# Kernel tuning notes

Measured on AMD Instinct MI355X. Metric: run time of the kernel, lower is better.

The kernel has to match this reference:

```python
import jax, jax.numpy as jnp
import numpy as np

N, IN_DIM, HID, HEADS = 4096, 256, 64, 8


def setup_inputs() -> dict:
    key = jax.random.key(0)
    ks = jax.random.split(key, 9)
    feats = jax.random.normal(ks[0], (N, IN_DIM), dtype=jnp.float32)
    adj = jax.random.bernoulli(ks[1], 0.01, (N, N)) | jnp.eye(N, dtype=bool)
    def lin(k, fin, fout):
        return jax.random.normal(k, (fin, fout), dtype=jnp.float32) / np.float32(np.sqrt(fin))
    return {
        "features": feats,
        "adjacency": adj,
        "W_in": lin(ks[2], IN_DIM, HID * HEADS),            # linear (no bias)
        "W_out": lin(ks[3], HID * HEADS, HID),              # out_proj
        "b_out": jnp.zeros((HID,), jnp.float32),
        "W_c1": lin(ks[4], HID * 2, HID),                   # classifier[1]
        "b_c1": jnp.zeros((HID,), jnp.float32),
        "W_c2": lin(ks[5], HID, 1),                         # classifier[3]
        "b_c2": jnp.zeros((1,), jnp.float32),
    }


def reference(features, adjacency, W_in, W_out, b_out, W_c1, b_c1, W_c2, b_c2):
    n = features.shape[0]
    # multi-head GAT: [H, N, D]
    proj = (features @ W_in).reshape(n, HEADS, HID).transpose(1, 0, 2)
    logits = jnp.einsum('hnd,hmd->hnm', proj, proj) / np.float32(np.sqrt(HID))
    logits = jnp.where(adjacency[None, :, :], logits, -jnp.inf)
    attn = jax.nn.softmax(logits, axis=-1)
    attended = jnp.einsum('hnm,hmd->hnd', attn, proj)
    attended = attended.transpose(1, 0, 2).reshape(n, HEADS * HID)
    node_states = attended @ W_out + b_out
    # memory_bank is None -> concat with zeros
    fused = jnp.concatenate([node_states, jnp.zeros_like(node_states)], axis=-1)
    h = jax.nn.gelu(fused, approximate=False) @ W_c1 + b_c1
    scores = (jax.nn.gelu(h, approximate=False) @ W_c2 + b_c2).squeeze(-1)
    # attention heatmap: masked row-normalized cosine similarity
    eps = np.float32(1e-8)
    norm = jnp.maximum(jnp.linalg.norm(node_states, axis=-1, keepdims=True), eps)
    xn = node_states / norm
    sim = jnp.where(adjacency, xn @ xn.T, 0.0)
    heatmap = sim / (sim.sum(axis=-1, keepdims=True) + eps)
    return scores, heatmap
```

## Files before the change

kernel.cpp:

```cpp
#include <hip/hip_runtime.h>
#include <math.h>

constexpr int NN    = 4096;
constexpr int INDIM = 256;
constexpr int HID   = 64;
constexpr int HEADS = 8;
constexpr int HH    = HID * HEADS;
constexpr int DMAX  = 256;
constexpr int PROJ_BLOCKS = 512;

typedef float        vfloat4 __attribute__((ext_vector_type(4)));
typedef unsigned int vuint4  __attribute__((ext_vector_type(4)));

__device__ __forceinline__ float gelu_exact(float x) {
    return 0.5f * x * (1.0f + erff(x * 0.70710678118654752f));
}

__device__ __forceinline__ float wave_reduce64(float v) {
    v += __shfl_xor(v, 32); v += __shfl_xor(v, 16); v += __shfl_xor(v, 8);
    v += __shfl_xor(v, 4);  v += __shfl_xor(v, 2);  v += __shfl_xor(v, 1);
    return v;
}

__global__ __launch_bounds__(256) void prep_kernel(
    const void* __restrict__ adjv,
    const float* __restrict__ A, const float* __restrict__ B,
    float* __restrict__ projT,
    unsigned short* __restrict__ nbr_g, int* __restrict__ deg_g) {
    __shared__ float Bs[64][64];
    __shared__ int wsum[4], u8w[4];
    const int pb = blockIdx.x, t = threadIdx.x;
    const int wv = t >> 6, lane = t & 63;

    if (pb < PROJ_BLOCKS) {
        const int bx = pb >> 6, by = pb & 63;
        const int tx = t & 15, ty = t >> 4;
        const float* ap0 = A + (size_t)(by * 64 + ty * 4 + 0) * INDIM;
        const float* ap1 = A + (size_t)(by * 64 + ty * 4 + 1) * INDIM;
        const float* ap2 = A + (size_t)(by * 64 + ty * 4 + 2) * INDIM;
        const float* ap3 = A + (size_t)(by * 64 + ty * 4 + 3) * INDIM;
        float acc[4][4] = {{0.0f}};

        for (int kq = 0; kq < 4; ++kq) {
            #pragma unroll
            for (int i = t; i < 64 * 16; i += 256) {
                const int k = i >> 4, c4 = (i & 15) * 4;
                *reinterpret_cast<float4*>(&Bs[k][c4]) =
                    *reinterpret_cast<const float4*>(
                        B + (size_t)(kq * 64 + k) * HH + bx * 64 + c4);
            }
            __syncthreads();
            #pragma unroll 2
            for (int k = 0; k < 64; k += 4) {
                const int ka = kq * 64 + k;
                float4 av[4];
                av[0] = *reinterpret_cast<const float4*>(ap0 + ka);
                av[1] = *reinterpret_cast<const float4*>(ap1 + ka);
                av[2] = *reinterpret_cast<const float4*>(ap2 + ka);
                av[3] = *reinterpret_cast<const float4*>(ap3 + ka);
                float4 bv[4];
                #pragma unroll
                for (int kk = 0; kk < 4; ++kk)
                    bv[kk] = *reinterpret_cast<const float4*>(&Bs[k + kk][tx * 4]);
                #pragma unroll
                for (int i = 0; i < 4; ++i) {
                    const float a0 = av[i].x, a1 = av[i].y, a2 = av[i].z, a3 = av[i].w;
                    acc[i][0] += a0 * bv[0].x + a1 * bv[1].x + a2 * bv[2].x + a3 * bv[3].x;
                    acc[i][1] += a0 * bv[0].y + a1 * bv[1].y + a2 * bv[2].y + a3 * bv[3].y;
                    acc[i][2] += a0 * bv[0].z + a1 * bv[1].z + a2 * bv[2].z + a3 * bv[3].z;
                    acc[i][3] += a0 * bv[0].w + a1 * bv[1].w + a2 * bv[2].w + a3 * bv[3].w;
                }
            }
            __syncthreads();
        }
        #pragma unroll
        for (int i = 0; i < 4; ++i) {
            float4 o = {acc[i][0], acc[i][1], acc[i][2], acc[i][3]};
            *reinterpret_cast<float4*>(
                projT + ((size_t)bx * NN + by * 64 + ty * 4 + i) * HID + tx * 4) = o;
        }
    } else {
        const int n = pb - PROJ_BLOCKS;
        const vuint4 r8 = __builtin_nontemporal_load(
            reinterpret_cast<const vuint4*>(
                (const unsigned char*)adjv + (size_t)n * NN + 16 * t));
        const vuint4 pw = *(reinterpret_cast<const vuint4*>(adjv) + t);
        int u8loc = 0;
        #pragma unroll
        for (int a = 0; a < 4; ++a) {
            const unsigned w = pw[a];
            if (((w & ~0x01010101u) == 0u) && ((w & 0xFFFFFF00u) != 0u)) u8loc = 1;
        }
        const unsigned long long wb = __ballot(u8loc);
        if (lane == 0) u8w[wv] = (wb != 0ull);
        __syncthreads();
        const bool isU8 = (u8w[0] | u8w[1] | u8w[2] | u8w[3]) != 0;

        unsigned int nzmask = 0;
        if (isU8) {
            #pragma unroll
            for (int a = 0; a < 4; ++a)
                #pragma unroll
                for (int j = 0; j < 4; ++j)
                    if ((r8[a] >> (8 * j)) & 0xFFu) nzmask |= 1u << (a * 4 + j);
        } else {
            const vuint4* p = reinterpret_cast<const vuint4*>(
                (const unsigned int*)adjv + (size_t)n * NN + 16 * t);
            #pragma unroll
            for (int a = 0; a < 4; ++a) {
                const vuint4 r = __builtin_nontemporal_load(p + a);
                if (r[0]) nzmask |= 1u << (a * 4 + 0);
                if (r[1]) nzmask |= 1u << (a * 4 + 1);
                if (r[2]) nzmask |= 1u << (a * 4 + 2);
                if (r[3]) nzmask |= 1u << (a * 4 + 3);
            }
        }
        const int c = __popc(nzmask);
        int x = c;
        #pragma unroll
        for (int d = 1; d < 64; d <<= 1) {
            int y = __shfl_up(x, d);
            if (lane >= d) x += y;
        }
        if (lane == 63) wsum[wv] = x;
        __syncthreads();
        int base = 0;
        #pragma unroll
        for (int i = 0; i < 4; ++i)
            if (i < wv) base += wsum[i];
        const int deg = min(wsum[0] + wsum[1] + wsum[2] + wsum[3], DMAX);
        if (t == 0) deg_g[n] = deg;
        int o = base + x - c;
        unsigned int mm = nzmask;
        while (mm) {
            const int j = __ffs(mm) - 1;
            mm &= mm - 1;
            if (o < DMAX) nbr_g[(size_t)n * DMAX + o] = (unsigned short)(16 * t + j);
            ++o;
        }
    }
}

__global__ __launch_bounds__(256) void attn_kernel(
    const float* __restrict__ projT,
    const unsigned short* __restrict__ nbr_g, const int* __restrict__ deg_g,
    float* __restrict__ attended) {
    __shared__ unsigned short nl[4][DMAX];
    const int b = blockIdx.x, t = threadIdx.x;
    const int wv = t >> 6, lane = t & 63;
    const int h = b & 7;
    const int n = (b >> 3) * 4 + wv;
    const int deg = deg_g[n];

    *reinterpret_cast<ushort4*>(&nl[wv][lane * 4]) =
        *reinterpret_cast<const ushort4*>(nbr_g + (size_t)n * DMAX + lane * 4);

    const float* tab = projT + (size_t)h * NN * HID;
    const int g = lane >> 3, dl = (lane & 7) * 8;

    float q[8];
    {
        const float4 a = *reinterpret_cast<const float4*>(tab + (size_t)n * HID + dl);
        const float4 bq = *reinterpret_cast<const float4*>(tab + (size_t)n * HID + dl + 4);
        q[0] = a.x;  q[1] = a.y;  q[2] = a.z;  q[3] = a.w;
        q[4] = bq.x; q[5] = bq.y; q[6] = bq.z; q[7] = bq.w;
    }

    float l = 0.0f;
    float acc[8] = {0.f, 0.f, 0.f, 0.f, 0.f, 0.f, 0.f, 0.f};
    for (int c0 = 0; c0 < deg; c0 += 8) {
        const int c = c0 + g;
        const int idx = nl[wv][min(c, deg - 1)];
        const float* kp = tab + (size_t)idx * HID + dl;
        const float4 ka = *reinterpret_cast<const float4*>(kp);
        const float4 kb = *reinterpret_cast<const float4*>(kp + 4);
        float kf[8] = {ka.x, ka.y, ka.z, ka.w, kb.x, kb.y, kb.z, kb.w};
        float s = q[0]*kf[0] + q[1]*kf[1] + q[2]*kf[2] + q[3]*kf[3] +
                  q[4]*kf[4] + q[5]*kf[5] + q[6]*kf[6] + q[7]*kf[7];
        s += __shfl_xor(s, 1); s += __shfl_xor(s, 2); s += __shfl_xor(s, 4);
        const float w = (c < deg) ? expf(s * 0.125f) : 0.0f;
        l += w;
        #pragma unroll
        for (int i = 0; i < 8; ++i) acc[i] += w * kf[i];
    }
    l += __shfl_xor(l, 8); l += __shfl_xor(l, 16); l += __shfl_xor(l, 32);
    #pragma unroll
    for (int i = 0; i < 8; ++i) {
        acc[i] += __shfl_xor(acc[i], 8);
        acc[i] += __shfl_xor(acc[i], 16);
        acc[i] += __shfl_xor(acc[i], 32);
    }
    const float invL = 1.0f / l;
    if (g == 0) {
        float4 o1 = {acc[0] * invL, acc[1] * invL, acc[2] * invL, acc[3] * invL};
        float4 o2 = {acc[4] * invL, acc[5] * invL, acc[6] * invL, acc[7] * invL};
        float* dst = attended + (size_t)n * HH + h * HID + dl;
        *reinterpret_cast<float4*>(dst)     = o1;
        *reinterpret_cast<float4*>(dst + 4) = o2;
    }
}

__global__ __launch_bounds__(256) void post_kernel(
    const float* __restrict__ attended,
    const float* __restrict__ W_out, const float* __restrict__ b_out,
    const float* __restrict__ W_c1, const float* __restrict__ b_c1,
    const float* __restrict__ W_c2, const float* __restrict__ b_c2,
    float* __restrict__ scores, float* __restrict__ xn) {
    __shared__ float qv2[4][HH];
    __shared__ float red[4][256];
    __shared__ float nsbuf[4][HID];
    const int n0 = blockIdx.x * 4, t = threadIdx.x;
    const int wv = t >> 6, lane = t & 63;

    #pragma unroll
    for (int nd = 0; nd < 4; ++nd) {
        qv2[nd][t]       = attended[(size_t)(n0 + nd) * HH + t];
        qv2[nd][t + 256] = attended[(size_t)(n0 + nd) * HH + t + 256];
    }
    __syncthreads();

    const int j = t & 63, part = t >> 6;
    float p0 = 0.f, p1 = 0.f, p2 = 0.f, p3 = 0.f;
    for (int d = part * 128; d < part * 128 + 128; ++d) {
        const float w = W_out[d * HID + j];
        p0 += qv2[0][d] * w; p1 += qv2[1][d] * w;
        p2 += qv2[2][d] * w; p3 += qv2[3][d] * w;
    }
    red[0][t] = p0; red[1][t] = p1; red[2][t] = p2; red[3][t] = p3;
    __syncthreads();
    if (wv < 4 && lane < HID) {
        nsbuf[wv][lane] = red[wv][lane] + red[wv][lane + 64] +
                          red[wv][lane + 128] + red[wv][lane + 192] + b_out[lane];
    }
    __syncthreads();

    const int n = n0 + wv;
    const float ns = nsbuf[wv][lane];
    const float s2 = wave_reduce64(ns * ns);
    const float invn = 1.0f / fmaxf(sqrtf(s2), 1e-8f);
    xn[(size_t)n * HID + lane] = ns * invn;
    const float gb = gelu_exact(ns);
    __syncthreads();
    nsbuf[wv][lane] = gb;
    float hv = b_c1[lane];
    for (int i = 0; i < HID; ++i) hv += nsbuf[wv][i] * W_c1[i * HID + lane];
    const float hb = gelu_exact(hv);
    const float sc_ = wave_reduce64(hb * W_c2[lane]);
    if (lane == 0) scores[n] = sc_ + b_c2[0];
}

__global__ __launch_bounds__(256, 8) void heat_kernel(
    const unsigned short* __restrict__ nbr_g, const int* __restrict__ deg_g,
    const float* __restrict__ xn, float* __restrict__ heat) {
    __shared__ float srow[NN];
    __shared__ float simv[DMAX];
    __shared__ unsigned short nl[DMAX];
    __shared__ float inv_s;
    const int n = blockIdx.x, t = threadIdx.x;
    const int wv = t >> 6, lane = t & 63;
    const int deg = deg_g[n];

    float4* sr4 = (float4*)srow;
    const float4 z4 = {0.f, 0.f, 0.f, 0.f};
    for (int i = t; i < NN / 4; i += 256) sr4[i] = z4;
    if (t < deg) nl[t] = nbr_g[(size_t)n * DMAX + t];
    const float xq = xn[(size_t)n * HID + lane];
    __syncthreads();

    for (int c = wv; c < deg; c += 4) {
        const int m = nl[c];
        float s = wave_reduce64(xq * xn[(size_t)m * HID + lane]);
        if (lane == 0) { srow[m] = s; simv[c] = s; }
    }
    __syncthreads();
    if (t < 64) {
        float ps = 0.0f;
        for (int c = t; c < deg; c += 64) ps += simv[c];
        ps = wave_reduce64(ps);
        if (t == 0) inv_s = 1.0f / (ps + 1e-8f);
    }
    __syncthreads();
    const float inv = inv_s;
    vfloat4* hr4 = (vfloat4*)(heat + (size_t)n * NN);
    for (int i = t; i < NN / 4; i += 256) {
        float4 v = sr4[i];
        vfloat4 nv = {v.x * inv, v.y * inv, v.z * inv, v.w * inv};
        __builtin_nontemporal_store(nv, hr4 + i);
    }
}

extern "C" void kernel_launch(void* const* d_in, const int* in_sizes, int n_in,
                              void* d_out, int out_size, void* d_ws, size_t ws_size,
                              hipStream_t stream) {
    const float* features = (const float*)d_in[0];
    const void*  adj      = d_in[1];
    const float* W_in     = (const float*)d_in[2];
    const float* W_out    = (const float*)d_in[3];
    const float* b_out    = (const float*)d_in[4];
    const float* W_c1     = (const float*)d_in[5];
    const float* b_c1     = (const float*)d_in[6];
    const float* W_c2     = (const float*)d_in[7];
    const float* b_c2     = (const float*)d_in[8];

    float* scores = (float*)d_out;
    float* heat   = (float*)d_out + NN;

    float*          projT    = (float*)d_ws;
    float*          attended = projT + (size_t)HEADS * NN * HID;
    float*          xn       = attended + (size_t)NN * HH;
    unsigned short* nbr_g    = (unsigned short*)(xn + (size_t)NN * HID);
    int*            deg_g    = (int*)(nbr_g + (size_t)NN * DMAX);

    prep_kernel<<<PROJ_BLOCKS + NN, 256, 0, stream>>>(adj, features, W_in,
                                                      projT, nbr_g, deg_g);
    attn_kernel<<<NN * HEADS / 4, 256, 0, stream>>>(projT, nbr_g, deg_g, attended);
    post_kernel<<<NN / 4, 256, 0, stream>>>(attended, W_out, b_out, W_c1, b_c1,
                                            W_c2, b_c2, scores, xn);
    heat_kernel<<<NN, 256, 0, stream>>>(nbr_g, deg_g, xn, heat);
}
```

Measured before the change: 220.4 us.

## Stage A tiles in LDS and register-prefetch next k-tile in projection GEMM

The projection GEMM in prep_kernel used to read A directly from global memory in the inner loop. It now stages the A tile in padded shared memory alongside B. The next k-slab of both A and B is prefetched into registers while the current slab is computed, so global load latency overlaps the FMAs. This costs extra LDS (about 17KB more) and register pressure, which could lower occupancy, and it only touches the projection part of a larger pipeline.

Result: slower. 225.1 us (+2.2%).

```diff
diff --git a/kernel.cpp b/kernel.cpp
--- a/kernel.cpp
+++ b/kernel.cpp
@@ -27,6 +27,7 @@
     const float* __restrict__ A, const float* __restrict__ B,
     float* __restrict__ projT,
     unsigned short* __restrict__ nbr_g, int* __restrict__ deg_g) {
+    __shared__ float As[64][68];
     __shared__ float Bs[64][64];
     __shared__ int wsum[4], u8w[4];
     const int pb = blockIdx.x, t = threadIdx.x;
@@ -35,30 +36,43 @@
     if (pb < PROJ_BLOCKS) {
         const int bx = pb >> 6, by = pb & 63;
         const int tx = t & 15, ty = t >> 4;
-        const float* ap0 = A + (size_t)(by * 64 + ty * 4 + 0) * INDIM;
-        const float* ap1 = A + (size_t)(by * 64 + ty * 4 + 1) * INDIM;
-        const float* ap2 = A + (size_t)(by * 64 + ty * 4 + 2) * INDIM;
-        const float* ap3 = A + (size_t)(by * 64 + ty * 4 + 3) * INDIM;
         float acc[4][4] = {{0.0f}};
 
+        float4 ar[4], br[4];
+        const int r_row[4] = {t >> 4, (t + 256) >> 4, (t + 512) >> 4, (t + 768) >> 4};
+        const int r_c4    = (t & 15) * 4;
+
+        #pragma unroll
+        for (int j = 0; j < 4; ++j) {
+            ar[j] = *reinterpret_cast<const float4*>(
+                A + (size_t)(by * 64 + r_row[j]) * INDIM + 0 * 64 + r_c4);
+            br[j] = *reinterpret_cast<const float4*>(
+                B + (size_t)(0 * 64 + r_row[j]) * HH + bx * 64 + r_c4);
+        }
+
         for (int kq = 0; kq < 4; ++kq) {
+            __syncthreads();
             #pragma unroll
-            for (int i = t; i < 64 * 16; i += 256) {
-                const int k = i >> 4, c4 = (i & 15) * 4;
-                *reinterpret_cast<float4*>(&Bs[k][c4]) =
-                    *reinterpret_cast<const float4*>(
-                        B + (size_t)(kq * 64 + k) * HH + bx * 64 + c4);
+            for (int j = 0; j < 4; ++j) {
+                *reinterpret_cast<float4*>(&As[r_row[j]][r_c4]) = ar[j];
+                *reinterpret_cast<float4*>(&Bs[r_row[j]][r_c4]) = br[j];
+            }
+            if (kq < 3) {
+                #pragma unroll
+                for (int j = 0; j < 4; ++j) {
+                    ar[j] = *reinterpret_cast<const float4*>(
+                        A + (size_t)(by * 64 + r_row[j]) * INDIM + (kq + 1) * 64 + r_c4);
+                    br[j] = *reinterpret_cast<const float4*>(
+                        B + (size_t)((kq + 1) * 64 + r_row[j]) * HH + bx * 64 + r_c4);
+                }
             }
             __syncthreads();
             #pragma unroll 2
             for (int k = 0; k < 64; k += 4) {
-                const int ka = kq * 64 + k;
-                float4 av[4];
-                av[0] = *reinterpret_cast<const float4*>(ap0 + ka);
-                av[1] = *reinterpret_cast<const float4*>(ap1 + ka);
-                av[2] = *reinterpret_cast<const float4*>(ap2 + ka);
-                av[3] = *reinterpret_cast<const float4*>(ap3 + ka);
-                float4 bv[4];
+                float4 av[4], bv[4];
+                #pragma unroll
+                for (int i = 0; i < 4; ++i)
+                    av[i] = *reinterpret_cast<const float4*>(&As[ty * 4 + i][k]);
                 #pragma unroll
                 for (int kk = 0; kk < 4; ++kk)
                     bv[kk] = *reinterpret_cast<const float4*>(&Bs[k + kk][tx * 4]);
@@ -71,7 +85,6 @@
                     acc[i][3] += a0 * bv[0].w + a1 * bv[1].w + a2 * bv[2].w + a3 * bv[3].w;
                 }
             }
-            __syncthreads();
         }
         #pragma unroll
         for (int i = 0; i < 4; ++i) {
```
